# Performance work log

Hardware: AMD Instinct MI355X
Metric: run time of the kernel (lower is better)

The kernel has to match this reference:

```python
import jax, jax.numpy as jnp
import numpy as np

B, N, T, E, H, R = 8, 64, 128, 128, 8, 4
DH = E // H


def setup_inputs() -> dict:
    key = jax.random.key(0)
    ks = jax.random.split(key, 14)
    s = 1.0 / np.sqrt(E)
    return {
        "node_memory": jax.random.normal(ks[0], (B, N, T, E), jnp.float32),
        "subgraph_memory": jax.random.normal(ks[1], (B, N, T, E, R - 1), jnp.float32),
        "Wq": jax.random.normal(ks[2], (E, E), jnp.float32) * s,
        "bq": jnp.zeros((E,), jnp.float32),
        "Wk": jax.random.normal(ks[3], (E, E), jnp.float32) * s,
        "bk": jnp.zeros((E,), jnp.float32),
        "Wv": jax.random.normal(ks[4], (E, E), jnp.float32) * s,
        "bv": jnp.zeros((E,), jnp.float32),
        "in_w": jax.random.normal(ks[5], (3 * E, E), jnp.float32) * s,
        "in_b": jnp.zeros((3 * E,), jnp.float32),
        "out_w": jax.random.normal(ks[6], (E, E), jnp.float32) * s,
        "out_b": jnp.zeros((E,), jnp.float32),
        "fc_w": jax.random.normal(ks[7], (E, R * E), jnp.float32) * (1.0 / np.sqrt(R * E)),
        "fc_b": jnp.zeros((E,), jnp.float32),
    }


def reference(node_memory, subgraph_memory, Wq, bq, Wk, bk, Wv, bv,
              in_w, in_b, out_w, out_b, fc_w, fc_b):
    # combined: [B,N,T,R,E] = concat(node[...,None,:], subgraph permuted)
    combined = jnp.concatenate(
        [node_memory[..., None, :], jnp.swapaxes(subgraph_memory, -1, -2)], axis=-2)
    # outer QKV projections
    Q = jnp.einsum("bntrf,ef->bntre", combined, Wq) + bq
    K = jnp.einsum("bntrf,ef->bntre", combined, Wk) + bk
    V = jnp.einsum("bntrf,ef->bntre", combined, Wv) + bv
    # nn.MultiheadAttention in-projection
    q = jnp.einsum("bntre,fe->bntrf", Q, in_w[:E]) + in_b[:E]
    k = jnp.einsum("bntre,fe->bntrf", K, in_w[E:2 * E]) + in_b[E:2 * E]
    v = jnp.einsum("bntre,fe->bntrf", V, in_w[2 * E:]) + in_b[2 * E:]
    # split heads: [B,N,T,R,H,DH]
    q = q.reshape(B, N, T, R, H, DH) * (1.0 / np.sqrt(DH))
    k = k.reshape(B, N, T, R, H, DH)
    v = v.reshape(B, N, T, R, H, DH)
    scores = jnp.einsum("bntrhd,bntshd->bnthrs", q, k)  # [B,N,T,H,R,R]
    attn = jax.nn.softmax(scores, axis=-1)
    o = jnp.einsum("bnthrs,bntshd->bntrhd", attn, v).reshape(B, N, T, R, E)
    o = jnp.einsum("bntre,fe->bntrf", o, out_w) + out_b
    # concat the R representations and fuse
    o = o.reshape(B, N, T, R * E)
    return jnp.einsum("bntc,ec->bnte", o, fc_w) + fc_b
```

## Files before the change

kernel.cpp:

```cpp
#include <hip/hip_runtime.h>
#include <hip/hip_bf16.h>

constexpr int cE  = 128;
constexpr int cR  = 4;
constexpr int cNT = 65536;

typedef short s8v  __attribute__((ext_vector_type(8)));
typedef unsigned short u8v __attribute__((ext_vector_type(8)));
typedef float f4v  __attribute__((ext_vector_type(4)));

static __device__ __forceinline__ unsigned short f2bf(float x) {
    union { float f; unsigned int u; } v; v.f = x;
    unsigned int r = v.u + 0x7fffu + ((v.u >> 16) & 1u);
    return (unsigned short)(r >> 16);
}
static __device__ __forceinline__ float bf2f(unsigned short u) {
    union { unsigned int u; float f; } v; v.u = ((unsigned int)u) << 16;
    return v.f;
}

__global__ __launch_bounds__(256) void k_prep(
    const float* __restrict__ Wq, const float* __restrict__ Wk, const float* __restrict__ Wv,
    const float* __restrict__ in_w, const float* __restrict__ out_w, const float* __restrict__ fc_w,
    const float* __restrict__ bq, const float* __restrict__ bk, const float* __restrict__ bv,
    const float* __restrict__ in_b, const float* __restrict__ out_b, const float* __restrict__ fc_b,
    unsigned short* __restrict__ wqkv, unsigned short* __restrict__ meff,
    float* __restrict__ bqkv, float* __restrict__ beff)
{
    int bid = blockIdx.x;
    if (bid < 1792) {
        int gt = bid * 256 + (int)threadIdx.x;
        int o  = gt >> 2;
        int p  = gt & 3;
        float s;
        if (o < 3 * cE * cE) {
            int w   = o >> 14;
            int rem = o & (cE * cE - 1);
            int f = rem >> 7, g = rem & 127;
            const float* Wsel = (w == 0) ? Wq : ((w == 1) ? Wk : Wv);
            const float* iw = in_w + (size_t)(w * cE + f) * cE + p * 32;
            const float* wp = Wsel + (size_t)(p * 32) * cE + g;
            float s0 = 0.f, s1 = 0.f;
            #pragma unroll
            for (int e = 0; e < 32; e += 2) {
                s0 += iw[e]     * wp[(size_t)e * cE];
                s1 += iw[e + 1] * wp[(size_t)(e + 1) * cE];
            }
            s = s0 + s1;
            s += __shfl_xor(s, 1);
            s += __shfl_xor(s, 2);
            if (w == 0) s *= 0.25f;
            if (p == 0) wqkv[o] = f2bf(s);
        } else {
            int i2 = o - 3 * cE * cE;
            int e1 = i2 >> 9;
            int c  = i2 & 511;
            const float* fw = fc_w + (size_t)e1 * 512 + (c >> 7) * cE + p * 32;
            int ee = c & 127;
            const float* ow = out_w + (size_t)(p * 32) * cE + ee;
            float s0 = 0.f, s1 = 0.f;
            #pragma unroll
            for (int ff = 0; ff < 32; ff += 2) {
                s0 += fw[ff]     * ow[(size_t)ff * cE];
                s1 += fw[ff + 1] * ow[(size_t)(ff + 1) * cE];
            }
            s = s0 + s1;
            s += __shfl_xor(s, 1);
            s += __shfl_xor(s, 2);
            if (p == 0) meff[i2] = f2bf(s);
        }
    } else {
        int idx = (bid - 1792) * 256 + (int)threadIdx.x;
        if (idx < 384) {
            int w = idx >> 7, f = idx & 127;
            const float* bsel = (w == 0) ? bq : ((w == 1) ? bk : bv);
            const float* iw = in_w + (size_t)(w * cE + f) * cE;
            float s = 0.f;
            for (int e = 0; e < cE; ++e) s += iw[e] * bsel[e];
            s += in_b[w * cE + f];
            if (w == 0) s *= 0.25f;
            bqkv[idx] = s;
        } else {
            int f = idx - 384;
            float s = 0.f;
            for (int c = 0; c < 512; ++c) s += fc_w[(size_t)f * 512 + c] * out_b[c & 127];
            beff[f] = s + fc_b[f];
        }
    }
}

#define TOKB   32
#define TOKC   8
#define PITCH  136
#define OPITCH 520

__global__ __launch_bounds__(256) void k_main(
    const float* __restrict__ node, const float* __restrict__ sub,
    const unsigned short* __restrict__ wqkv,
    const unsigned short* __restrict__ meff,
    const float* __restrict__ bqkv,
    const float* __restrict__ beff,
    float* __restrict__ out)
{
    __shared__ unsigned short uAO[32 * PITCH];
    __shared__ unsigned short sQKV[3][cR * TOKC][PITCH];
    __shared__ float sBias[3 * cE];

    const int tid  = threadIdx.x;
    const int lane = tid & 63;
    const int wv   = tid >> 6;
    const int l15  = lane & 15;
    const int lq   = lane >> 4;
    const int ct0  = wv * 2;

    for (int i = tid; i < 3 * cE; i += 256) sBias[i] = bqkv[i];

    const int tokBlock = blockIdx.x * TOKB;

    for (int chunk = 0; chunk < TOKB / TOKC; ++chunk) {
        const int tokBase = tokBlock + chunk * TOKC;
        __syncthreads();

        {
            int tok = tid >> 5;
            int e4  = (tid & 31) * 4;
            float4 v = *(const float4*)(node + (size_t)(tokBase + tok) * cE + e4);
            *(ushort4*)&uAO[(tok * cR) * PITCH + e4] =
                make_ushort4(f2bf(v.x), f2bf(v.y), f2bf(v.z), f2bf(v.w));
        }
        {
            int tok = tid >> 5;
            int eg  = tid & 31;
            const float* sp = sub + (size_t)(tokBase + tok) * 384 + eg * 12;
            float4 f0 = *(const float4*)(sp + 0);
            float4 f1 = *(const float4*)(sp + 4);
            float4 f2 = *(const float4*)(sp + 8);
            int e0 = eg * 4;
            *(ushort4*)&uAO[(tok * cR + 1) * PITCH + e0] =
                make_ushort4(f2bf(f0.x), f2bf(f0.w), f2bf(f1.z), f2bf(f2.y));
            *(ushort4*)&uAO[(tok * cR + 2) * PITCH + e0] =
                make_ushort4(f2bf(f0.y), f2bf(f1.x), f2bf(f1.w), f2bf(f2.z));
            *(ushort4*)&uAO[(tok * cR + 3) * PITCH + e0] =
                make_ushort4(f2bf(f0.z), f2bf(f1.y), f2bf(f2.x), f2bf(f2.w));
        }
        __syncthreads();

        for (int w = 0; w < 3; ++w) {
            const unsigned short* wbase = wqkv + (size_t)w * cE * cE;
            f4v acc[2][2];
            #pragma unroll
            for (int a = 0; a < 2; ++a)
                #pragma unroll
                for (int b = 0; b < 2; ++b) acc[a][b] = (f4v){0.f, 0.f, 0.f, 0.f};
            #pragma unroll
            for (int kc = 0; kc < 4; ++kc) {
                int koff = kc * 32 + lq * 8;
                s8v a0 = *(const s8v*)&uAO[(0 * 16 + l15) * PITCH + koff];
                s8v a1 = *(const s8v*)&uAO[(1 * 16 + l15) * PITCH + koff];
                #pragma unroll
                for (int c = 0; c < 2; ++c) {
                    int f = (ct0 + c) * 16 + l15;
                    s8v b = *(const s8v*)(wbase + (size_t)f * cE + koff);
                    acc[0][c] = __builtin_amdgcn_mfma_f32_16x16x32_bf16(b, a0, acc[0][c], 0, 0, 0);
                    acc[1][c] = __builtin_amdgcn_mfma_f32_16x16x32_bf16(b, a1, acc[1][c], 0, 0, 0);
                }
            }
            #pragma unroll
            for (int rt = 0; rt < 2; ++rt)
                #pragma unroll
                for (int c = 0; c < 2; ++c) {
                    int col = (ct0 + c) * 16 + lq * 4;
                    float4 b4 = *(const float4*)&sBias[w * cE + col];
                    *(ushort4*)&sQKV[w][rt * 16 + l15][col] =
                        make_ushort4(f2bf(acc[rt][c][0] + b4.x),
                                     f2bf(acc[rt][c][1] + b4.y),
                                     f2bf(acc[rt][c][2] + b4.z),
                                     f2bf(acc[rt][c][3] + b4.w));
                }
        }
        __syncthreads();

        {
            int tok = tid >> 5;
            int h   = (tid >> 2) & 7;
            int r   = tid & 3;
            const unsigned short* qp = &sQKV[0][tok * cR + r][h * 16];
            u8v q0 = *(const u8v*)qp, q1 = *(const u8v*)(qp + 8);
            float q[16];
            #pragma unroll
            for (int d = 0; d < 8; ++d) { q[d] = bf2f(q0[d]); q[8 + d] = bf2f(q1[d]); }
            float sc[4];
            #pragma unroll
            for (int s = 0; s < 4; ++s) {
                const unsigned short* kp = &sQKV[1][tok * cR + s][h * 16];
                u8v k0 = *(const u8v*)kp, k1 = *(const u8v*)(kp + 8);
                float t = 0.f;
                #pragma unroll
                for (int d = 0; d < 8; ++d) t += q[d] * bf2f(k0[d]) + q[8 + d] * bf2f(k1[d]);
                sc[s] = t;
            }
            float m = fmaxf(fmaxf(sc[0], sc[1]), fmaxf(sc[2], sc[3]));
            float p[4], l = 0.f;
            #pragma unroll
            for (int s = 0; s < 4; ++s) { p[s] = __expf(sc[s] - m); l += p[s]; }
            float inv = 1.f / l;
            float o[16];
            #pragma unroll
            for (int d = 0; d < 16; ++d) o[d] = 0.f;
            #pragma unroll
            for (int s = 0; s < 4; ++s) {
                float w = p[s] * inv;
                const unsigned short* vp = &sQKV[2][tok * cR + s][h * 16];
                u8v v0 = *(const u8v*)vp, v1 = *(const u8v*)(vp + 8);
                #pragma unroll
                for (int d = 0; d < 8; ++d) { o[d] += w * bf2f(v0[d]); o[8 + d] += w * bf2f(v1[d]); }
            }
            unsigned int pk[8];
            #pragma unroll
            for (int d2 = 0; d2 < 8; ++d2)
                pk[d2] = (unsigned int)f2bf(o[2 * d2]) | ((unsigned int)f2bf(o[2 * d2 + 1]) << 16);
            uint4* op = (uint4*)&uAO[tok * OPITCH + r * cE + h * 16];
            op[0] = make_uint4(pk[0], pk[1], pk[2], pk[3]);
            op[1] = make_uint4(pk[4], pk[5], pk[6], pk[7]);
        }
        __syncthreads();

        {
            f4v acc[2];
            acc[0] = (f4v){0.f, 0.f, 0.f, 0.f};
            acc[1] = (f4v){0.f, 0.f, 0.f, 0.f};
            int arow = l15 & 7;
            #pragma unroll 4
            for (int kc = 0; kc < 16; ++kc) {
                int koff = kc * 32 + lq * 8;
                s8v a = *(const s8v*)&uAO[arow * OPITCH + koff];
                #pragma unroll
                for (int c = 0; c < 2; ++c) {
                    int e1 = (ct0 + c) * 16 + l15;
                    s8v b = *(const s8v*)(meff + (size_t)e1 * 512 + koff);
                    acc[c] = __builtin_amdgcn_mfma_f32_16x16x32_bf16(b, a, acc[c], 0, 0, 0);
                }
            }
            if (l15 < 8) {
                size_t tokOff = (size_t)(tokBase + l15) * cE;
                #pragma unroll
                for (int c = 0; c < 2; ++c) {
                    int col = (ct0 + c) * 16 + lq * 4;
                    float4 b4 = *(const float4*)&beff[col];
                    *(float4*)&out[tokOff + col] =
                        make_float4(acc[c][0] + b4.x, acc[c][1] + b4.y,
                                    acc[c][2] + b4.z, acc[c][3] + b4.w);
                }
            }
        }
    }
}

extern "C" void kernel_launch(void* const* d_in, const int* in_sizes, int n_in,
                              void* d_out, int out_size, void* d_ws, size_t ws_size,
                              hipStream_t stream) {
    const float* node  = (const float*)d_in[0];
    const float* sub   = (const float*)d_in[1];
    const float* Wq    = (const float*)d_in[2];
    const float* bq    = (const float*)d_in[3];
    const float* Wk    = (const float*)d_in[4];
    const float* bk    = (const float*)d_in[5];
    const float* Wv    = (const float*)d_in[6];
    const float* bv    = (const float*)d_in[7];
    const float* in_w  = (const float*)d_in[8];
    const float* in_b  = (const float*)d_in[9];
    const float* out_w = (const float*)d_in[10];
    const float* out_b = (const float*)d_in[11];
    const float* fc_w  = (const float*)d_in[12];
    const float* fc_b  = (const float*)d_in[13];

    unsigned short* ws_wqkv = (unsigned short*)d_ws;
    unsigned short* ws_meff = ws_wqkv + 3 * cE * cE;
    float* ws_bqkv = (float*)((char*)d_ws + (size_t)(3 * cE * cE + cE * cR * cE) * 2);
    float* ws_beff = ws_bqkv + 3 * cE;

    k_prep<<<dim3(1794), dim3(256), 0, stream>>>(Wq, Wk, Wv, in_w, out_w, fc_w,
                                                 bq, bk, bv, in_b, out_b, fc_b,
                                                 ws_wqkv, ws_meff, ws_bqkv, ws_beff);
    k_main<<<dim3(cNT / TOKB), dim3(256), 0, stream>>>(node, sub, ws_wqkv, ws_meff,
                                                       ws_bqkv, ws_beff, (float*)d_out);
}
```

Before: 347.8 us.

## Compute attention in registers from MFMA accumulators via DPP and shuffles

```diff
diff --git a/kernel.cpp b/kernel.cpp
--- a/kernel.cpp
+++ b/kernel.cpp
@@ -6,7 +6,6 @@
 constexpr int cNT = 65536;
 
 typedef short s8v  __attribute__((ext_vector_type(8)));
-typedef unsigned short u8v __attribute__((ext_vector_type(8)));
 typedef float f4v  __attribute__((ext_vector_type(4)));
 
 static __device__ __forceinline__ unsigned short f2bf(float x) {
@@ -14,10 +13,9 @@
     unsigned int r = v.u + 0x7fffu + ((v.u >> 16) & 1u);
     return (unsigned short)(r >> 16);
 }
-static __device__ __forceinline__ float bf2f(unsigned short u) {
-    union { unsigned int u; float f; } v; v.u = ((unsigned int)u) << 16;
-    return v.f;
-}
+
+#define QB(x, C) __int_as_float(__builtin_amdgcn_update_dpp( \
+            0, __float_as_int(x), C, 0xF, 0xF, false))
 
 __global__ __launch_bounds__(256) void k_prep(
     const float* __restrict__ Wq, const float* __restrict__ Wk, const float* __restrict__ Wv,
@@ -103,8 +101,6 @@
     float* __restrict__ out)
 {
     __shared__ unsigned short uAO[32 * PITCH];
-    __shared__ unsigned short sQKV[3][cR * TOKC][PITCH];
-    __shared__ float sBias[3 * cE];
 
     const int tid  = threadIdx.x;
     const int lane = tid & 63;
@@ -112,8 +108,6 @@
     const int l15  = lane & 15;
     const int lq   = lane >> 4;
     const int ct0  = wv * 2;
-
-    for (int i = tid; i < 3 * cE; i += 256) sBias[i] = bqkv[i];
 
     const int tokBlock = blockIdx.x * TOKB;
 
@@ -145,83 +139,91 @@
         }
         __syncthreads();
 
-        for (int w = 0; w < 3; ++w) {
-            const unsigned short* wbase = wqkv + (size_t)w * cE * cE;
-            f4v acc[2][2];
-            #pragma unroll
-            for (int a = 0; a < 2; ++a)
+        f4v qa[2][2], ka[2][2], va[2][2];
+        #pragma unroll
+        for (int rt = 0; rt < 2; ++rt)
+            #pragma unroll
+            for (int cc = 0; cc < 2; ++cc) {
+                qa[rt][cc] = (f4v){0.f, 0.f, 0.f, 0.f};
+                ka[rt][cc] = (f4v){0.f, 0.f, 0.f, 0.f};
+                va[rt][cc] = (f4v){0.f, 0.f, 0.f, 0.f};
+            }
+        #pragma unroll
+        for (int kc = 0; kc < 4; ++kc) {
+            const int koff = kc * 32 + lq * 8;
+            s8v a0 = *(const s8v*)&uAO[l15 * PITCH + koff];
+            s8v a1 = *(const s8v*)&uAO[(16 + l15) * PITCH + koff];
+            #pragma unroll
+            for (int cc = 0; cc < 2; ++cc) {
+                const size_t fo = (size_t)((ct0 + cc) * 16 + l15) * cE + koff;
+                s8v wq_ = *(const s8v*)(wqkv + fo);
+                s8v wk_ = *(const s8v*)(wqkv + 16384 + fo);
+                s8v wv_ = *(const s8v*)(wqkv + 32768 + fo);
+                qa[0][cc] = __builtin_amdgcn_mfma_f32_16x16x32_bf16(wq_, a0, qa[0][cc], 0, 0, 0);
+                qa[1][cc] = __builtin_amdgcn_mfma_f32_16x16x32_bf16(wq_, a1, qa[1][cc], 0, 0, 0);
+                ka[0][cc] = __builtin_amdgcn_mfma_f32_16x16x32_bf16(wk_, a0, ka[0][cc], 0, 0, 0);
+                ka[1][cc] = __builtin_amdgcn_mfma_f32_16x16x32_bf16(wk_, a1, ka[1][cc], 0, 0, 0);
+                va[0][cc] = __builtin_amdgcn_mfma_f32_16x16x32_bf16(wv_, a0, va[0][cc], 0, 0, 0);
+                va[1][cc] = __builtin_amdgcn_mfma_f32_16x16x32_bf16(wv_, a1, va[1][cc], 0, 0, 0);
+            }
+        }
+        #pragma unroll
+        for (int cc = 0; cc < 2; ++cc) {
+            const int fb = (ct0 + cc) * 16 + lq * 4;
+            float4 b0 = *(const float4*)(bqkv + fb);
+            float4 b1 = *(const float4*)(bqkv + cE + fb);
+            float4 b2 = *(const float4*)(bqkv + 2 * cE + fb);
+            #pragma unroll
+            for (int rt = 0; rt < 2; ++rt) {
+                qa[rt][cc][0] += b0.x; qa[rt][cc][1] += b0.y;
+                qa[rt][cc][2] += b0.z; qa[rt][cc][3] += b0.w;
+                ka[rt][cc][0] += b1.x; ka[rt][cc][1] += b1.y;
+                ka[rt][cc][2] += b1.z; ka[rt][cc][3] += b1.w;
+                va[rt][cc][0] += b2.x; va[rt][cc][1] += b2.y;
+                va[rt][cc][2] += b2.z; va[rt][cc][3] += b2.w;
+            }
+        }
+
+        __syncthreads();
+
+        {
+            const int r  = l15 & 3;
+            const int tq = l15 >> 2;
+            #pragma unroll
+            for (int rt = 0; rt < 2; ++rt) {
                 #pragma unroll
-                for (int b = 0; b < 2; ++b) acc[a][b] = (f4v){0.f, 0.f, 0.f, 0.f};
-            #pragma unroll
-            for (int kc = 0; kc < 4; ++kc) {
-                int koff = kc * 32 + lq * 8;
-                s8v a0 = *(const s8v*)&uAO[(0 * 16 + l15) * PITCH + koff];
-                s8v a1 = *(const s8v*)&uAO[(1 * 16 + l15) * PITCH + koff];
-                #pragma unroll
-                for (int c = 0; c < 2; ++c) {
-                    int f = (ct0 + c) * 16 + l15;
-                    s8v b = *(const s8v*)(wbase + (size_t)f * cE + koff);
-                    acc[0][c] = __builtin_amdgcn_mfma_f32_16x16x32_bf16(b, a0, acc[0][c], 0, 0, 0);
-                    acc[1][c] = __builtin_amdgcn_mfma_f32_16x16x32_bf16(b, a1, acc[1][c], 0, 0, 0);
+                for (int cc = 0; cc < 2; ++cc) {
+                    f4v q = qa[rt][cc], k = ka[rt][cc], v = va[rt][cc];
+                    float s0 = QB(k[0],0x00)*q[0] + QB(k[1],0x00)*q[1]
+                             + QB(k[2],0x00)*q[2] + QB(k[3],0x00)*q[3];
+                    float s1 = QB(k[0],0x55)*q[0] + QB(k[1],0x55)*q[1]
+                             + QB(k[2],0x55)*q[2] + QB(k[3],0x55)*q[3];
+                    float s2 = QB(k[0],0xAA)*q[0] + QB(k[1],0xAA)*q[1]
+                             + QB(k[2],0xAA)*q[2] + QB(k[3],0xAA)*q[3];
+                    float s3 = QB(k[0],0xFF)*q[0] + QB(k[1],0xFF)*q[1]
+                             + QB(k[2],0xFF)*q[2] + QB(k[3],0xFF)*q[3];
+                    s0 += __shfl_xor(s0, 16); s0 += __shfl_xor(s0, 32);
+                    s1 += __shfl_xor(s1, 16); s1 += __shfl_xor(s1, 32);
+                    s2 += __shfl_xor(s2, 16); s2 += __shfl_xor(s2, 32);
+                    s3 += __shfl_xor(s3, 16); s3 += __shfl_xor(s3, 32);
+                    float m = fmaxf(fmaxf(s0, s1), fmaxf(s2, s3));
+                    float p0 = __expf(s0 - m), p1 = __expf(s1 - m);
+                    float p2 = __expf(s2 - m), p3 = __expf(s3 - m);
+                    float inv = 1.f / (p0 + p1 + p2 + p3);
+                    p0 *= inv; p1 *= inv; p2 *= inv; p3 *= inv;
+                    float o0 = p0*QB(v[0],0x00) + p1*QB(v[0],0x55)
+                             + p2*QB(v[0],0xAA) + p3*QB(v[0],0xFF);
+                    float o1 = p0*QB(v[1],0x00) + p1*QB(v[1],0x55)
+                             + p2*QB(v[1],0xAA) + p3*QB(v[1],0xFF);
+                    float o2 = p0*QB(v[2],0x00) + p1*QB(v[2],0x55)
+                             + p2*QB(v[2],0xAA) + p3*QB(v[2],0xFF);
+                    float o3 = p0*QB(v[3],0x00) + p1*QB(v[3],0x55)
+                             + p2*QB(v[3],0xAA) + p3*QB(v[3],0xFF);
+                    int tok = rt * 4 + tq;
+                    *(ushort4*)&uAO[tok * OPITCH + r * cE + (ct0 + cc) * 16 + lq * 4] =
+                        make_ushort4(f2bf(o0), f2bf(o1), f2bf(o2), f2bf(o3));
                 }
             }
-            #pragma unroll
-            for (int rt = 0; rt < 2; ++rt)
-                #pragma unroll
-                for (int c = 0; c < 2; ++c) {
-                    int col = (ct0 + c) * 16 + lq * 4;
-                    float4 b4 = *(const float4*)&sBias[w * cE + col];
-                    *(ushort4*)&sQKV[w][rt * 16 + l15][col] =
-                        make_ushort4(f2bf(acc[rt][c][0] + b4.x),
-                                     f2bf(acc[rt][c][1] + b4.y),
-                                     f2bf(acc[rt][c][2] + b4.z),
-                                     f2bf(acc[rt][c][3] + b4.w));
-                }
-        }
-        __syncthreads();
-
-        {
-            int tok = tid >> 5;
-            int h   = (tid >> 2) & 7;
-            int r   = tid & 3;
-            const unsigned short* qp = &sQKV[0][tok * cR + r][h * 16];
-            u8v q0 = *(const u8v*)qp, q1 = *(const u8v*)(qp + 8);
-            float q[16];
-            #pragma unroll
-            for (int d = 0; d < 8; ++d) { q[d] = bf2f(q0[d]); q[8 + d] = bf2f(q1[d]); }
-            float sc[4];
-            #pragma unroll
-            for (int s = 0; s < 4; ++s) {
-                const unsigned short* kp = &sQKV[1][tok * cR + s][h * 16];
-                u8v k0 = *(const u8v*)kp, k1 = *(const u8v*)(kp + 8);
-                float t = 0.f;
-                #pragma unroll
-                for (int d = 0; d < 8; ++d) t += q[d] * bf2f(k0[d]) + q[8 + d] * bf2f(k1[d]);
-                sc[s] = t;
-            }
-            float m = fmaxf(fmaxf(sc[0], sc[1]), fmaxf(sc[2], sc[3]));
-            float p[4], l = 0.f;
-            #pragma unroll
-            for (int s = 0; s < 4; ++s) { p[s] = __expf(sc[s] - m); l += p[s]; }
-            float inv = 1.f / l;
-            float o[16];
-            #pragma unroll
-            for (int d = 0; d < 16; ++d) o[d] = 0.f;
-            #pragma unroll
-            for (int s = 0; s < 4; ++s) {
-                float w = p[s] * inv;
-                const unsigned short* vp = &sQKV[2][tok * cR + s][h * 16];
-                u8v v0 = *(const u8v*)vp, v1 = *(const u8v*)(vp + 8);
-                #pragma unroll
-                for (int d = 0; d < 8; ++d) { o[d] += w * bf2f(v0[d]); o[8 + d] += w * bf2f(v1[d]); }
-            }
-            unsigned int pk[8];
-            #pragma unroll
-            for (int d2 = 0; d2 < 8; ++d2)
-                pk[d2] = (unsigned int)f2bf(o[2 * d2]) | ((unsigned int)f2bf(o[2 * d2 + 1]) << 16);
-            uint4* op = (uint4*)&uAO[tok * OPITCH + r * cE + h * 16];
-            op[0] = make_uint4(pk[0], pk[1], pk[2], pk[3]);
-            op[1] = make_uint4(pk[4], pk[5], pk[6], pk[7]);
         }
         __syncthreads();
 
```

Measured after the change: 348.6 us. About the same (+0.2%).
